# Kernel optimization log

Measured on AMD Instinct MI355X. Metric: run time of the kernel, lower is better.

The kernel has to match this reference:

```python
import jax, jax.numpy as jnp
import numpy as np

N_TOKENS = 16384
D_IN = 1024
D_HID = 4096
D_OUT = 1024
N_EXPERTS = 8


def setup_inputs() -> dict:
    key = jax.random.key(0)
    ks = jax.random.split(key, 7)
    s_in = 1.0 / np.sqrt(D_IN)
    s_hid = 1.0 / np.sqrt(D_HID)
    return {
        "x": jax.random.normal(ks[0], (N_TOKENS, D_IN), dtype=jnp.float32),
        "Wr": jax.random.uniform(ks[1], (D_IN, N_EXPERTS), jnp.float32, -s_in, s_in),
        "br": jax.random.uniform(ks[2], (N_EXPERTS,), jnp.float32, -s_in, s_in),
        "W1": jax.random.uniform(ks[3], (N_EXPERTS, D_IN, D_HID), jnp.float32, -s_in, s_in),
        "b1": jax.random.uniform(ks[4], (N_EXPERTS, D_HID), jnp.float32, -s_in, s_in),
        "W2": jax.random.uniform(ks[5], (N_EXPERTS, D_HID, D_OUT), jnp.float32, -s_hid, s_hid),
        "b2": jax.random.uniform(ks[6], (N_EXPERTS, D_OUT), jnp.float32, -s_hid, s_hid),
    }


def reference(x, Wr, br, W1, b1, W2, b2):
    # Router: softmax over expert logits, hard top-1 dispatch (argmax).
    # Note: output is NOT scaled by routing probs in the original module.
    logits = x @ Wr + br                      # [N, E]
    expert_idx = jnp.argmax(logits, axis=-1)  # [N] (argmax of softmax == argmax of logits)

    n_experts = W1.shape[0]
    out = jnp.zeros((x.shape[0], W2.shape[-1]), dtype=x.dtype)
    # world_size=1 -> all_to_all is identity; masked per-expert dense FFN + combine.
    # Fixed small loop over experts (structurally distinct weights), vectorized over tokens.
    for e in range(n_experts):
        mask = (expert_idx == e)[:, None]                 # [N, 1]
        xe = jnp.where(mask, x, 0.0)                      # zero out tokens not routed here
        y = jax.nn.relu(xe @ W1[e] + b1[e]) @ W2[e] + b2[e]  # [N, D_OUT]
        out = jnp.where(mask, y, out)
    return out
```

## Files before the change

kernel.cpp:

```cpp
#include <hip/hip_runtime.h>
#include <cstdint>

#define NT   16384
#define DIN  1024
#define DHID 4096
#define DOUT 1024
#define NE   8

typedef unsigned short u16;
typedef short bf16x8 __attribute__((ext_vector_type(8)));
typedef float f32x4  __attribute__((ext_vector_type(4)));

__device__ __forceinline__ u16 f2b(float f) {
  union { float f; unsigned u; } a; a.f = f;
  unsigned u = a.u;
  return (u16)((u + 0x7FFFu + ((u >> 16) & 1u)) >> 16);
}

__device__ __forceinline__ void gl_lds16(const u16* g, u16* l) {
  __builtin_amdgcn_global_load_lds(
      (const __attribute__((address_space(1))) void*)g,
      (__attribute__((address_space(3))) void*)l,
      16, 0, 0);
}

__global__ void router_kernel(const float* __restrict__ x, const float* __restrict__ Wr,
                              const float* __restrict__ br, u16* __restrict__ Xb,
                              int* __restrict__ eidx, int* __restrict__ counts) {
  int t = blockIdx.x * 4 + (threadIdx.x >> 6);
  int lane = threadIdx.x & 63;
  const float* xr = x + (size_t)t * DIN;
  u16* xbr = Xb + (size_t)t * DIN;
  float acc[NE];
#pragma unroll
  for (int e = 0; e < NE; e++) acc[e] = 0.f;
#pragma unroll
  for (int i = 0; i < DIN / 64; i++) {
    int k = lane + i * 64;
    float xv = xr[k];
    xbr[k] = f2b(xv);
    const float4 w0 = *(const float4*)(Wr + (size_t)k * NE);
    const float4 w1 = *(const float4*)(Wr + (size_t)k * NE + 4);
    acc[0] += xv * w0.x; acc[1] += xv * w0.y; acc[2] += xv * w0.z; acc[3] += xv * w0.w;
    acc[4] += xv * w1.x; acc[5] += xv * w1.y; acc[6] += xv * w1.z; acc[7] += xv * w1.w;
  }
#pragma unroll
  for (int off = 32; off > 0; off >>= 1) {
#pragma unroll
    for (int e = 0; e < NE; e++) acc[e] += __shfl_down(acc[e], off, 64);
  }
  if (lane == 0) {
    int best = 0; float bv = acc[0] + br[0];
#pragma unroll
    for (int e = 1; e < NE; e++) {
      float v = acc[e] + br[e];
      if (v > bv) { bv = v; best = e; }
    }
    eidx[t] = best;
    atomicAdd(&counts[best], 1);
  }
}

__global__ void zero_kernel(int* __restrict__ p) {
  if (threadIdx.x < 16) p[threadIdx.x] = 0;
}

__global__ void scan_kernel(const int* __restrict__ counts, int* __restrict__ offsets) {
  if (threadIdx.x == 0) {
    int s = 0;
    for (int e = 0; e < NE; e++) { offsets[e] = s; s += counts[e]; }
    offsets[NE] = s;
  }
}

__global__ void scatter_kernel(const int* __restrict__ eidx, const int* __restrict__ offsets,
                               int* __restrict__ cursor, int* __restrict__ perm) {
  int t = blockIdx.x * blockDim.x + threadIdx.x;
  if (t >= NT) return;
  int e = eidx[t];
  int pos = offsets[e] + atomicAdd(&cursor[e], 1);
  perm[pos] = t;
}

__global__ void transpose_cvt_kernel(const float* __restrict__ W, u16* __restrict__ Wt,
                                     int K, int H) {
  __shared__ float tile[64][65];
  const int e = blockIdx.z;
  const int k0 = blockIdx.x * 64, h0 = blockIdx.y * 64;
  const float* src = W + (size_t)e * K * H;
  u16* dst = Wt + (size_t)e * K * H;
  const int tid = threadIdx.x;
#pragma unroll
  for (int i = 0; i < 4; i++) {
    int idx = tid + i * 256;
    int r = idx >> 4;
    int c = (idx & 15) * 4;
    const float4 v = *(const float4*)(src + (size_t)(k0 + r) * H + h0 + c);
    tile[r][c] = v.x; tile[r][c + 1] = v.y; tile[r][c + 2] = v.z; tile[r][c + 3] = v.w;
  }
  __syncthreads();
#pragma unroll
  for (int i = 0; i < 4; i++) {
    int idx = tid + i * 256;
    int r = idx >> 4;
    int c = (idx & 15) * 4;
    ushort4 o;
    o.x = f2b(tile[c][r]); o.y = f2b(tile[c + 1][r]);
    o.z = f2b(tile[c + 2][r]); o.w = f2b(tile[c + 3][r]);
    *(ushort4*)(dst + (size_t)(h0 + r) * K + k0 + c) = o;
  }
}

template<bool GATHER_A, bool STORE_HIDDEN>
__global__ __launch_bounds__(256, 2) void moe_gemm(
    const u16* __restrict__ A, const u16* __restrict__ Bt,
    const float* __restrict__ bias,
    const int* __restrict__ perm, const int* __restrict__ counts,
    const int* __restrict__ offsets,
    u16* __restrict__ Hout, float* __restrict__ Fout,
    int K, int N) {
  const int e = blockIdx.z;
  const int cnt = counts[e];
  const int m0 = blockIdx.y * 128;
  if (m0 >= cnt) return;
  int valid = cnt - m0; if (valid > 128) valid = 128;
  const int base_p = offsets[e] + m0;
  const int n0 = blockIdx.x * 128;

  __shared__ u16 sA[128 * 32];
  __shared__ u16 sB[128 * 32];

  const int tid = threadIdx.x;
  const int lane = tid & 63;
  const int wave = tid >> 6;
  const int wm = (wave >> 1) * 64;
  const int wn = (wave & 1) * 64;
  const int quad = lane >> 4;
  const int l15 = lane & 15;

  const int rr = lane >> 2;
  const int cb = (lane & 3) * 8;

  const int rA0 = wave * 16 + rr;
  const int rA1 = rA0 + 64;

  int pa0 = base_p + rA0; if (pa0 > NT - 1) pa0 = NT - 1;
  int pa1 = base_p + rA1; if (pa1 > NT - 1) pa1 = NT - 1;
  const int arow0 = GATHER_A ? perm[pa0] : pa0;
  const int arow1 = GATHER_A ? perm[pa1] : pa1;
  const u16* aptr0 = A + (size_t)arow0 * K + cb;
  const u16* aptr1 = A + (size_t)arow1 * K + cb;
  const u16* bptr0 = Bt + ((size_t)e * N + n0 + rA0) * K + cb;
  const u16* bptr1 = Bt + ((size_t)e * N + n0 + rA1) * K + cb;

  u16* dA0 = &sA[wave * 512];
  u16* dA1 = &sA[wave * 512 + 2048];
  u16* dB0 = &sB[wave * 512];
  u16* dB1 = &sB[wave * 512 + 2048];

  f32x4 acc[4][4];
#pragma unroll
  for (int mi = 0; mi < 4; mi++)
#pragma unroll
    for (int ni = 0; ni < 4; ni++)
      acc[mi][ni] = (f32x4){0.f, 0.f, 0.f, 0.f};

  const int kiters = K >> 5;
  for (int kt = 0; kt < kiters; kt++) {
    if (kt) __syncthreads();
    gl_lds16(aptr0, dA0);
    gl_lds16(aptr1, dA1);
    gl_lds16(bptr0, dB0);
    gl_lds16(bptr1, dB1);
    aptr0 += 32; aptr1 += 32; bptr0 += 32; bptr1 += 32;
    __syncthreads();

    bf16x8 af[4], bfr[4];
#pragma unroll
    for (int mi = 0; mi < 4; mi++)
      af[mi] = *(const bf16x8*)&sA[(wm + mi * 16 + l15) * 32 + quad * 8];
#pragma unroll
    for (int ni = 0; ni < 4; ni++)
      bfr[ni] = *(const bf16x8*)&sB[(wn + ni * 16 + l15) * 32 + quad * 8];
#pragma unroll
    for (int mi = 0; mi < 4; mi++)
#pragma unroll
      for (int ni = 0; ni < 4; ni++)
        acc[mi][ni] = __builtin_amdgcn_mfma_f32_16x16x32_bf16(af[mi], bfr[ni], acc[mi][ni], 0, 0, 0);
  }

  float bv[4];
#pragma unroll
  for (int ni = 0; ni < 4; ni++)
    bv[ni] = bias[(size_t)e * N + n0 + wn + ni * 16 + l15];

#pragma unroll
  for (int mi = 0; mi < 4; mi++) {
#pragma unroll
    for (int r = 0; r < 4; r++) {
      const int ml = wm + mi * 16 + quad * 4 + r;
      if (ml >= valid) continue;
      const int pp = base_p + ml;
      if (STORE_HIDDEN) {
        u16* orow = Hout + (size_t)pp * N + n0 + wn;
#pragma unroll
        for (int ni = 0; ni < 4; ni++) {
          float v = acc[mi][ni][r] + bv[ni];
          v = v > 0.f ? v : 0.f;
          orow[ni * 16 + l15] = f2b(v);
        }
      } else {
        const int token = perm[pp];
        float* orow = Fout + (size_t)token * N + n0 + wn;
#pragma unroll
        for (int ni = 0; ni < 4; ni++)
          orow[ni * 16 + l15] = acc[mi][ni][r] + bv[ni];
      }
    }
  }
}

__global__ void sentinel_kernel(float* __restrict__ out, int n) {
  int i = blockIdx.x * blockDim.x + threadIdx.x;
  if (i < n) out[i] = 31337.0f;
}

extern "C" void kernel_launch(void* const* d_in, const int* in_sizes, int n_in,
                              void* d_out, int out_size, void* d_ws, size_t ws_size,
                              hipStream_t stream) {
  const float* x  = (const float*)d_in[0];
  const float* Wr = (const float*)d_in[1];
  const float* br = (const float*)d_in[2];
  const float* W1 = (const float*)d_in[3];
  const float* b1 = (const float*)d_in[4];
  const float* W2 = (const float*)d_in[5];
  const float* b2 = (const float*)d_in[6];
  float* out = (float*)d_out;

  const size_t szXb  = (size_t)NT * DIN * 2;
  const size_t szW1t = (size_t)NE * DIN * DHID * 2;
  const size_t szW2t = (size_t)NE * DHID * DOUT * 2;
  const size_t szHid = (size_t)NT * DHID * 2;
  char* ws = (char*)d_ws;
  u16* Xb   = (u16*)ws;
  u16* W1t  = (u16*)(ws + szXb);
  u16* W2t  = (u16*)(ws + szXb + szW1t);
  u16* Hid  = (u16*)(ws + szXb + szW1t + szW2t);
  int* perm = (int*)(ws + szXb + szW1t + szW2t + szHid);
  int* eidx = perm + NT;
  int* ctrl = eidx + NT;
  int* counts  = ctrl;
  int* cursor  = ctrl + 8;
  int* offsets = ctrl + 16;
  const size_t NEED = szXb + szW1t + szW2t + szHid + (size_t)NT * 4 * 2 + 256;

  if (ws_size < NEED) {
    sentinel_kernel<<<(out_size + 255) / 256, 256, 0, stream>>>(out, out_size);
    return;
  }

  zero_kernel<<<1, 64, 0, stream>>>(ctrl);
  transpose_cvt_kernel<<<dim3(DIN / 64, DHID / 64, NE), 256, 0, stream>>>(W1, W1t, DIN, DHID);
  transpose_cvt_kernel<<<dim3(DHID / 64, DOUT / 64, NE), 256, 0, stream>>>(W2, W2t, DHID, DOUT);
  router_kernel<<<NT / 4, 256, 0, stream>>>(x, Wr, br, Xb, eidx, counts);
  scan_kernel<<<1, 64, 0, stream>>>(counts, offsets);
  scatter_kernel<<<NT / 256, 256, 0, stream>>>(eidx, offsets, cursor, perm);

  moe_gemm<true, true><<<dim3(DHID / 128, NT / 128, NE), 256, 0, stream>>>(
      Xb, W1t, b1, perm, counts, offsets, Hid, nullptr, DIN, DHID);
  moe_gemm<false, false><<<dim3(DOUT / 128, NT / 128, NE), 256, 0, stream>>>(
      Hid, W2t, b2, perm, counts, offsets, nullptr, out, DHID, DOUT);
}
```

Before: 1.066 ms.

## Compact MoE GEMM grid with a tile list and double the K step per iteration

The scan kernel now writes a compact list of (expert, offset, valid) M-tiles, so the GEMM grid covers at most 136 real tiles instead of launching 8x128 blocks where most exit immediately. Each main-loop iteration now loads two 32-wide K slabs into double-sized LDS and runs two MFMA passes, halving the number of barriers per K. The occupancy hint of 2 blocks per CU is removed from the launch bounds. The cost is twice the LDS per block, which may lower occupancy, and a serial tile-building loop in the single-thread scan.

```diff
diff --git a/kernel.cpp b/kernel.cpp
--- a/kernel.cpp
+++ b/kernel.cpp
@@ -6,6 +6,7 @@
 #define DHID 4096
 #define DOUT 1024
 #define NE   8
+#define NMT  136
 
 typedef unsigned short u16;
 typedef short bf16x8 __attribute__((ext_vector_type(8)));
@@ -65,11 +66,21 @@
   if (threadIdx.x < 16) p[threadIdx.x] = 0;
 }
 
-__global__ void scan_kernel(const int* __restrict__ counts, int* __restrict__ offsets) {
+__global__ void scan_kernel(const int* __restrict__ counts, int* __restrict__ offsets,
+                            int4* __restrict__ tiles) {
   if (threadIdx.x == 0) {
-    int s = 0;
-    for (int e = 0; e < NE; e++) { offsets[e] = s; s += counts[e]; }
+    int s = 0, nt = 0;
+    for (int e = 0; e < NE; e++) {
+      int c = counts[e];
+      offsets[e] = s;
+      for (int m0 = 0; m0 < c; m0 += 128) {
+        int v = c - m0; if (v > 128) v = 128;
+        tiles[nt++] = make_int4(e, s + m0, v, 0);
+      }
+      s += c;
+    }
     offsets[NE] = s;
+    while (nt < NMT) tiles[nt++] = make_int4(0, 0, 0, 0);
   }
 }
 
@@ -112,23 +123,21 @@
 }
 
 template<bool GATHER_A, bool STORE_HIDDEN>
-__global__ __launch_bounds__(256, 2) void moe_gemm(
+__global__ __launch_bounds__(256) void moe_gemm(
     const u16* __restrict__ A, const u16* __restrict__ Bt,
     const float* __restrict__ bias,
-    const int* __restrict__ perm, const int* __restrict__ counts,
-    const int* __restrict__ offsets,
+    const int* __restrict__ perm, const int4* __restrict__ tiles,
     u16* __restrict__ Hout, float* __restrict__ Fout,
     int K, int N) {
-  const int e = blockIdx.z;
-  const int cnt = counts[e];
-  const int m0 = blockIdx.y * 128;
-  if (m0 >= cnt) return;
-  int valid = cnt - m0; if (valid > 128) valid = 128;
-  const int base_p = offsets[e] + m0;
+  const int4 ti = tiles[blockIdx.y];
+  const int valid = ti.z;
+  if (valid == 0) return;
+  const int e = ti.x;
+  const int base_p = ti.y;
   const int n0 = blockIdx.x * 128;
 
-  __shared__ u16 sA[128 * 32];
-  __shared__ u16 sB[128 * 32];
+  __shared__ u16 sA[2 * 128 * 32];
+  __shared__ u16 sB[2 * 128 * 32];
 
   const int tid = threadIdx.x;
   const int lane = tid & 63;
@@ -165,28 +174,35 @@
     for (int ni = 0; ni < 4; ni++)
       acc[mi][ni] = (f32x4){0.f, 0.f, 0.f, 0.f};
 
-  const int kiters = K >> 5;
+  const int kiters = K >> 6;
   for (int kt = 0; kt < kiters; kt++) {
     if (kt) __syncthreads();
-    gl_lds16(aptr0, dA0);
-    gl_lds16(aptr1, dA1);
-    gl_lds16(bptr0, dB0);
-    gl_lds16(bptr1, dB1);
-    aptr0 += 32; aptr1 += 32; bptr0 += 32; bptr1 += 32;
+    gl_lds16(aptr0,      dA0);
+    gl_lds16(aptr1,      dA1);
+    gl_lds16(bptr0,      dB0);
+    gl_lds16(bptr1,      dB1);
+    gl_lds16(aptr0 + 32, dA0 + 4096);
+    gl_lds16(aptr1 + 32, dA1 + 4096);
+    gl_lds16(bptr0 + 32, dB0 + 4096);
+    gl_lds16(bptr1 + 32, dB1 + 4096);
+    aptr0 += 64; aptr1 += 64; bptr0 += 64; bptr1 += 64;
     __syncthreads();
 
-    bf16x8 af[4], bfr[4];
-#pragma unroll
-    for (int mi = 0; mi < 4; mi++)
-      af[mi] = *(const bf16x8*)&sA[(wm + mi * 16 + l15) * 32 + quad * 8];
-#pragma unroll
-    for (int ni = 0; ni < 4; ni++)
-      bfr[ni] = *(const bf16x8*)&sB[(wn + ni * 16 + l15) * 32 + quad * 8];
-#pragma unroll
-    for (int mi = 0; mi < 4; mi++)
+#pragma unroll
+    for (int h = 0; h < 2; h++) {
+      bf16x8 af[4], bfr[4];
+#pragma unroll
+      for (int mi = 0; mi < 4; mi++)
+        af[mi] = *(const bf16x8*)&sA[h * 4096 + (wm + mi * 16 + l15) * 32 + quad * 8];
 #pragma unroll
       for (int ni = 0; ni < 4; ni++)
-        acc[mi][ni] = __builtin_amdgcn_mfma_f32_16x16x32_bf16(af[mi], bfr[ni], acc[mi][ni], 0, 0, 0);
+        bfr[ni] = *(const bf16x8*)&sB[h * 4096 + (wn + ni * 16 + l15) * 32 + quad * 8];
+#pragma unroll
+      for (int mi = 0; mi < 4; mi++)
+#pragma unroll
+        for (int ni = 0; ni < 4; ni++)
+          acc[mi][ni] = __builtin_amdgcn_mfma_f32_16x16x32_bf16(af[mi], bfr[ni], acc[mi][ni], 0, 0, 0);
+    }
   }
 
   float bv[4];
@@ -252,7 +268,8 @@
   int* counts  = ctrl;
   int* cursor  = ctrl + 8;
   int* offsets = ctrl + 16;
-  const size_t NEED = szXb + szW1t + szW2t + szHid + (size_t)NT * 4 * 2 + 256;
+  int4* tiles  = (int4*)(ctrl + 32);
+  const size_t NEED = szXb + szW1t + szW2t + szHid + (size_t)NT * 4 * 2 + 4096;
 
   if (ws_size < NEED) {
     sentinel_kernel<<<(out_size + 255) / 256, 256, 0, stream>>>(out, out_size);
@@ -263,11 +280,11 @@
   transpose_cvt_kernel<<<dim3(DIN / 64, DHID / 64, NE), 256, 0, stream>>>(W1, W1t, DIN, DHID);
   transpose_cvt_kernel<<<dim3(DHID / 64, DOUT / 64, NE), 256, 0, stream>>>(W2, W2t, DHID, DOUT);
   router_kernel<<<NT / 4, 256, 0, stream>>>(x, Wr, br, Xb, eidx, counts);
-  scan_kernel<<<1, 64, 0, stream>>>(counts, offsets);
+  scan_kernel<<<1, 64, 0, stream>>>(counts, offsets, tiles);
   scatter_kernel<<<NT / 256, 256, 0, stream>>>(eidx, offsets, cursor, perm);
 
-  moe_gemm<true, true><<<dim3(DHID / 128, NT / 128, NE), 256, 0, stream>>>(
-      Xb, W1t, b1, perm, counts, offsets, Hid, nullptr, DIN, DHID);
-  moe_gemm<false, false><<<dim3(DOUT / 128, NT / 128, NE), 256, 0, stream>>>(
-      Hid, W2t, b2, perm, counts, offsets, nullptr, out, DHID, DOUT);
-}
+  moe_gemm<true, true><<<dim3(DHID / 128, NMT), 256, 0, stream>>>(
+      Xb, W1t, b1, perm, tiles, Hid, nullptr, DIN, DHID);
+  moe_gemm<false, false><<<dim3(DOUT / 128, NMT), 256, 0, stream>>>(
+      Hid, W2t, b2, perm, tiles, nullptr, out, DHID, DOUT);
+}
```

After: 1.015 ms. 1.05x faster.
